# Optimization experiments

Measured on AMD Instinct MI355X. Metric: run time of the kernel, lower is better.

Reference implementation:

```python
import jax, jax.numpy as jnp
import numpy as np
from functools import partial

NX, NY = 48, 48
LX, LY = 1.0, 1.0
T, DT = 0.01, 0.0001
NT = int(T / DT)  # 100 sequential explicit-Euler steps
DX, DY = LX / NX, LY / NY
TWO_PI = 2.0 * jnp.pi


def setup_inputs() -> dict:
    key = jax.random.key(0)
    u0 = jax.random.normal(key, (8192, 1, NX, NY), dtype=jnp.float32)
    return {
        "u0": u0,
        "alpha_w1": jnp.float32(0.1),
        "alpha_w2": jnp.float32(0.1),
        "alpha_w3": jnp.float32(0.1),
        "beta_w1": jnp.float32(0.3),
        "beta_w2": jnp.float32(0.2),
        "beta_w3": jnp.float32(0.1),
    }


def _coeff_grids(a1, a2, a3, b1, b2, b3):
    x = jnp.linspace(0.0, LX, NX)
    y = jnp.linspace(0.0, LY, NY)
    yy, xx = jnp.meshgrid(y, x, indexing="ij")  # (NY, NX), matches torch.meshgrid(y, x, 'ij')
    alpha = 0.5 * DT * (jnp.abs(a1) + jnp.abs(a2) * jnp.sin(TWO_PI * yy)
                        + jnp.abs(a3) * jnp.cos(TWO_PI * yy)) / DX ** 2
    beta = DT * (jnp.abs(b1) + jnp.abs(b2) * jnp.cos(TWO_PI * xx)
                 + jnp.abs(b3) * jnp.sin(TWO_PI * xx)) / DY ** 2
    return alpha[None], beta[None]  # (1, NY, NX) broadcast over batch (square grid)


def reference(u0, alpha_w1, alpha_w2, alpha_w3, beta_w1, beta_w2, beta_w3):
    alpha_grid, beta_grid = _coeff_grids(alpha_w1, alpha_w2, alpha_w3,
                                         beta_w1, beta_w2, beta_w3)
    u = u0[:, 0]  # (B, NX, NY)
    # reflect-pad once; the boundary ring stays frozen across all timesteps
    u = jnp.pad(u, ((0, 0), (1, 1), (1, 1)), mode="reflect")

    def step(u, _):
        ui = u[:, 1:-1, 1:-1]
        u_xx = u[:, 2:, 1:-1] - 2.0 * ui + u[:, :-2, 1:-1]
        u_yy = u[:, 1:-1, 2:] - 2.0 * ui + u[:, 1:-1, :-2]
        u = u.at[:, 1:-1, 1:-1].set(ui + alpha_grid * u_xx + beta_grid * u_yy)
        return u, None

    u, _ = jax.lax.scan(step, u, None, length=NT)
    return u[:, 1:-1, 1:-1][:, None]  # (B, 1, NX, NY)
```

## Files before the change

kernel.cpp:

```cpp
#include <hip/hip_runtime.h>
#include <hip/hip_fp16.h>
#include <math.h>


#define NTSTEPS 100

typedef __half2 h2;

__device__ __forceinline__ h2 dpp_row_shr1(h2 oldv, h2 x) {
    int r = __builtin_amdgcn_update_dpp(
        __builtin_bit_cast(int, oldv), __builtin_bit_cast(int, x),
        0x111, 0xF, 0xF, false);
    return __builtin_bit_cast(h2, r);
}
__device__ __forceinline__ h2 dpp_row_shl1(h2 oldv, h2 x) {
    int r = __builtin_amdgcn_update_dpp(
        __builtin_bit_cast(int, oldv), __builtin_bit_cast(int, x),
        0x101, 0xF, 0xF, false);
    return __builtin_bit_cast(h2, r);
}
__device__ __forceinline__ h2 bperm(int addr, h2 x) {
    int r = __builtin_amdgcn_ds_bpermute(addr, __builtin_bit_cast(int, x));
    return __builtin_bit_cast(h2, r);
}

__global__ void coeff_kernel(
    const float* __restrict__ pa1, const float* __restrict__ pa2,
    const float* __restrict__ pa3, const float* __restrict__ pb1,
    const float* __restrict__ pb2, const float* __restrict__ pb3,
    float* __restrict__ ws)
{
    int tid = threadIdx.x;
    if (tid < 48) {
        float a1 = fabsf(pa1[0]), a2 = fabsf(pa2[0]), a3 = fabsf(pa3[0]);
        float b1 = fabsf(pb1[0]), b2 = fabsf(pb2[0]), b3 = fabsf(pb3[0]);
        float t = 6.283185307179586f * ((float)tid / 47.0f);
        float s = sinf(t), c = cosf(t);
        ws[tid]      = 0.1152f * (a1 + a2 * s + a3 * c);
        ws[48 + tid] = 0.2304f * (b1 + b2 * c + b3 * s);
    }
}

__global__ __launch_bounds__(256) void pde_kernel(
    const float* __restrict__ u0,
    const float* __restrict__ cw,
    float* __restrict__ out)
{
    const int tid  = threadIdx.x;
    const int lane = tid & 63;
    const int wv   = tid >> 6;
    const int pair = blockIdx.x * 4 + wv;
    const int tx   = lane & 15;
    const int ty   = lane >> 4;
    const int c0   = 3 * tx;
    const int r0   = 12 * ty;

    const float* __restrict__ srcA = u0 + (size_t)(2 * pair) * 2304;
    const float* __restrict__ srcB = srcA + 2304;

    h2 a[12], b[3];
    #pragma unroll
    for (int k = 0; k < 12; ++k) a[k] = __half2half2(__float2half(cw[r0 + k]));
    #pragma unroll
    for (int c = 0; c < 3; ++c) b[c] = __half2half2(__float2half(cw[48 + c0 + c]));
    const h2 neg2 = __floats2half2_rn(-2.0f, -2.0f);

    h2 u[12][3];
    h2 ep[12];
    h2 tH[3], bH[3];

    const int epc = (tx == 15) ? 46 : 1;
    #pragma unroll
    for (int k = 0; k < 12; ++k) {
        #pragma unroll
        for (int c = 0; c < 3; ++c) {
            int o = (r0 + k) * 48 + c0 + c;
            u[k][c] = __floats2half2_rn(srcA[o], srcB[o]);
        }
        int oe = (r0 + k) * 48 + epc;
        ep[k] = __floats2half2_rn(srcA[oe], srcB[oe]);
    }
    {
        const int tor = (ty == 0) ? 1 : (r0 - 1);
        const int bor = (ty == 3) ? 46 : (r0 + 12);
        #pragma unroll
        for (int c = 0; c < 3; ++c) {
            int ot = tor * 48 + c0 + c, ob = bor * 48 + c0 + c;
            tH[c] = __floats2half2_rn(srcA[ot], srcB[ot]);
            bH[c] = __floats2half2_rn(srcA[ob], srcB[ob]);
        }
    }

    const int upA = ((lane - 16) & 63) << 2;
    const int dnA = ((lane + 16) & 63) << 2;
    const bool notTop = (ty != 0);
    const bool notBot = (ty != 3);

    #pragma unroll 1
    for (int t = 0; t < NTSTEPS; ++t) {
        #pragma unroll
        for (int c = 0; c < 3; ++c) {
            h2 tv = bperm(upA, u[11][c]);
            h2 bv = bperm(dnA, u[0][c]);
            tH[c] = notTop ? tv : tH[c];
            bH[c] = notBot ? bv : bH[c];
        }
        h2 p0 = tH[0], p1 = tH[1], p2 = tH[2];
        #pragma unroll
        for (int k = 0; k < 12; ++k) {
            const h2 x0 = u[k][0], x1 = u[k][1], x2 = u[k][2];
            const h2 hl = dpp_row_shr1(ep[k], x2);
            const h2 hr = dpp_row_shl1(ep[k], x0);
            const h2 d0 = (k == 11) ? bH[0] : u[k + 1][0];
            const h2 d1 = (k == 11) ? bH[1] : u[k + 1][1];
            const h2 d2 = (k == 11) ? bH[2] : u[k + 1][2];
            const h2 s10 = __hadd2(p0, d0);
            const h2 s11 = __hadd2(p1, d1);
            const h2 s12 = __hadd2(p2, d2);
            const h2 s20 = __hadd2(hl, x1);
            const h2 s21 = __hadd2(x0, x2);
            const h2 s22 = __hadd2(x1, hr);
            const h2 t10 = __hfma2(neg2, x0, s10);
            const h2 t11 = __hfma2(neg2, x1, s11);
            const h2 t12 = __hfma2(neg2, x2, s12);
            const h2 t20 = __hfma2(neg2, x0, s20);
            const h2 t21 = __hfma2(neg2, x1, s21);
            const h2 t22 = __hfma2(neg2, x2, s22);
            const h2 n0 = __hfma2(b[0], t20, __hfma2(a[k], t10, x0));
            const h2 n1 = __hfma2(b[1], t21, __hfma2(a[k], t11, x1));
            const h2 n2 = __hfma2(b[2], t22, __hfma2(a[k], t12, x2));
            p0 = x0; p1 = x1; p2 = x2;
            u[k][0] = n0; u[k][1] = n1; u[k][2] = n2;
        }
    }

    float* __restrict__ dstA = out + (size_t)(2 * pair) * 2304;
    float* __restrict__ dstB = dstA + 2304;
    #pragma unroll
    for (int k = 0; k < 12; ++k) {
        #pragma unroll
        for (int c = 0; c < 3; ++c) {
            int o = (r0 + k) * 48 + c0 + c;
            dstA[o] = __low2float(u[k][c]);
            dstB[o] = __high2float(u[k][c]);
        }
    }
}

extern "C" void kernel_launch(void* const* d_in, const int* in_sizes, int n_in,
                              void* d_out, int out_size, void* d_ws, size_t ws_size,
                              hipStream_t stream) {
    const float* u0 = (const float*)d_in[0];
    float* ws = (float*)d_ws;
    coeff_kernel<<<1, 64, 0, stream>>>(
        (const float*)d_in[1], (const float*)d_in[2], (const float*)d_in[3],
        (const float*)d_in[4], (const float*)d_in[5], (const float*)d_in[6],
        ws);
    pde_kernel<<<1024, 256, 0, stream>>>(u0, ws, (float*)d_out);
}
```

Baseline: 335.7 us.

## Fold stencil diagonal into precomputed coefficients and overlap halo exchange with interior rows

Each update is rewritten as cc*x + a*(up+down) + b*(left+right), with the diagonal coefficient 1-2a-2b precomputed per cell. This removes the two -2x FMAs per row group. The frozen left and right boundary contributions are folded into per-row additive terms, so the DPP shifts can use zero-fill instead of old values. Boundary rows 0 and 11 are computed first and their ds_bpermute halo exchange is issued before the interior rows, hiding LDS-permute latency behind the interior arithmetic. The cost is more register pressure from the cc, e0 and e2 arrays, and changed fp16 rounding.

```diff
diff --git a/kernel.cpp b/kernel.cpp
--- a/kernel.cpp
+++ b/kernel.cpp
@@ -7,16 +7,14 @@
 
 typedef __half2 h2;
 
-__device__ __forceinline__ h2 dpp_row_shr1(h2 oldv, h2 x) {
+__device__ __forceinline__ h2 dpp_shr1_z(h2 x) {
     int r = __builtin_amdgcn_update_dpp(
-        __builtin_bit_cast(int, oldv), __builtin_bit_cast(int, x),
-        0x111, 0xF, 0xF, false);
+        0, __builtin_bit_cast(int, x), 0x111, 0xF, 0xF, true);
     return __builtin_bit_cast(h2, r);
 }
-__device__ __forceinline__ h2 dpp_row_shl1(h2 oldv, h2 x) {
+__device__ __forceinline__ h2 dpp_shl1_z(h2 x) {
     int r = __builtin_amdgcn_update_dpp(
-        __builtin_bit_cast(int, oldv), __builtin_bit_cast(int, x),
-        0x101, 0xF, 0xF, false);
+        0, __builtin_bit_cast(int, x), 0x101, 0xF, 0xF, true);
     return __builtin_bit_cast(h2, r);
 }
 __device__ __forceinline__ h2 bperm(int addr, h2 x) {
@@ -41,6 +39,21 @@
     }
 }
 
+#define ROWSTEP(K, UP0, UP1, UP2, DN0, DN1, DN2, X0, X1, X2, N0, N1, N2)      \
+    do {                                                                      \
+        const h2 hl  = dpp_shr1_z(X2);                                        \
+        const h2 hr  = dpp_shl1_z(X0);                                        \
+        const h2 s10 = __hadd2(UP0, DN0);                                     \
+        const h2 s11 = __hadd2(UP1, DN1);                                     \
+        const h2 s12 = __hadd2(UP2, DN2);                                     \
+        const h2 s20 = __hadd2(hl, X1);                                       \
+        const h2 s21 = __hadd2(X0, X2);                                       \
+        const h2 s22 = __hadd2(X1, hr);                                       \
+        N0 = __hfma2(a[K], s10, __hfma2(b0, s20, __hfma2(cc[K][0], X0, e0[K]))); \
+        N1 = __hfma2(a[K], s11, __hfma2(b1, s21, __hmul2(cc[K][1], X1)));     \
+        N2 = __hfma2(a[K], s12, __hfma2(b2, s22, __hfma2(cc[K][2], X2, e2[K]))); \
+    } while (0)
+
 __global__ __launch_bounds__(256) void pde_kernel(
     const float* __restrict__ u0,
     const float* __restrict__ cw,
@@ -58,17 +71,29 @@
     const float* __restrict__ srcA = u0 + (size_t)(2 * pair) * 2304;
     const float* __restrict__ srcB = srcA + 2304;
 
-    h2 a[12], b[3];
+    float bf0 = cw[48 + c0 + 0];
+    float bf1 = cw[48 + c0 + 1];
+    float bf2 = cw[48 + c0 + 2];
+    const h2 b0 = __half2half2(__float2half(bf0));
+    const h2 b1 = __half2half2(__float2half(bf1));
+    const h2 b2 = __half2half2(__float2half(bf2));
+
+    h2 a[12], cc[12][3];
     #pragma unroll
-    for (int k = 0; k < 12; ++k) a[k] = __half2half2(__float2half(cw[r0 + k]));
-    #pragma unroll
-    for (int c = 0; c < 3; ++c) b[c] = __half2half2(__float2half(cw[48 + c0 + c]));
-    const h2 neg2 = __floats2half2_rn(-2.0f, -2.0f);
+    for (int k = 0; k < 12; ++k) {
+        float av = cw[r0 + k];
+        a[k] = __half2half2(__float2half(av));
+        cc[k][0] = __half2half2(__float2half(1.0f - 2.0f * av - 2.0f * bf0));
+        cc[k][1] = __half2half2(__float2half(1.0f - 2.0f * av - 2.0f * bf1));
+        cc[k][2] = __half2half2(__float2half(1.0f - 2.0f * av - 2.0f * bf2));
+    }
 
     h2 u[12][3];
-    h2 ep[12];
+    h2 e0[12], e2[12];
     h2 tH[3], bH[3];
+    h2 tF[3], bF[3];
 
+    const h2 hz = __floats2half2_rn(0.0f, 0.0f);
     const int epc = (tx == 15) ? 46 : 1;
     #pragma unroll
     for (int k = 0; k < 12; ++k) {
@@ -78,7 +103,9 @@
             u[k][c] = __floats2half2_rn(srcA[o], srcB[o]);
         }
         int oe = (r0 + k) * 48 + epc;
-        ep[k] = __floats2half2_rn(srcA[oe], srcB[oe]);
+        float eA = srcA[oe], eB = srcB[oe];
+        e0[k] = (tx == 0)  ? __floats2half2_rn(bf0 * eA, bf0 * eB) : hz;
+        e2[k] = (tx == 15) ? __floats2half2_rn(bf2 * eA, bf2 * eB) : hz;
     }
     {
         const int tor = (ty == 0) ? 1 : (r0 - 1);
@@ -88,6 +115,8 @@
             int ot = tor * 48 + c0 + c, ob = bor * 48 + c0 + c;
             tH[c] = __floats2half2_rn(srcA[ot], srcB[ot]);
             bH[c] = __floats2half2_rn(srcA[ob], srcB[ob]);
+            tF[c] = tH[c];
+            bF[c] = bH[c];
         }
     }
 
@@ -98,39 +127,46 @@
 
     #pragma unroll 1
     for (int t = 0; t < NTSTEPS; ++t) {
+        h2 n0, n1, n2;
+        const h2 x110 = u[11][0], x111 = u[11][1], x112 = u[11][2];
+        ROWSTEP(11, u[10][0], u[10][1], u[10][2], bH[0], bH[1], bH[2],
+                x110, x111, x112, n0, n1, n2);
+        u[11][0] = n0; u[11][1] = n1; u[11][2] = n2;
+
+        h2 p0 = u[0][0], p1 = u[0][1], p2 = u[0][2];
+        ROWSTEP(0, tH[0], tH[1], tH[2], u[1][0], u[1][1], u[1][2],
+                p0, p1, p2, n0, n1, n2);
+        u[0][0] = n0; u[0][1] = n1; u[0][2] = n2;
+
+        const bool more = (t + 1 < NTSTEPS);
+        h2 rT0, rT1, rT2, rB0, rB1, rB2;
+        if (more) {
+            rT0 = bperm(upA, u[11][0]);
+            rT1 = bperm(upA, u[11][1]);
+            rT2 = bperm(upA, u[11][2]);
+            rB0 = bperm(dnA, u[0][0]);
+            rB1 = bperm(dnA, u[0][1]);
+            rB2 = bperm(dnA, u[0][2]);
+        }
+
         #pragma unroll
-        for (int c = 0; c < 3; ++c) {
-            h2 tv = bperm(upA, u[11][c]);
-            h2 bv = bperm(dnA, u[0][c]);
-            tH[c] = notTop ? tv : tH[c];
-            bH[c] = notBot ? bv : bH[c];
+        for (int k = 1; k <= 10; ++k) {
+            const h2 q0 = u[k][0], q1 = u[k][1], q2 = u[k][2];
+            const h2 d0 = (k == 10) ? x110 : u[k + 1][0];
+            const h2 d1 = (k == 10) ? x111 : u[k + 1][1];
+            const h2 d2 = (k == 10) ? x112 : u[k + 1][2];
+            ROWSTEP(k, p0, p1, p2, d0, d1, d2, q0, q1, q2, n0, n1, n2);
+            u[k][0] = n0; u[k][1] = n1; u[k][2] = n2;
+            p0 = q0; p1 = q1; p2 = q2;
         }
-        h2 p0 = tH[0], p1 = tH[1], p2 = tH[2];
-        #pragma unroll
-        for (int k = 0; k < 12; ++k) {
-            const h2 x0 = u[k][0], x1 = u[k][1], x2 = u[k][2];
-            const h2 hl = dpp_row_shr1(ep[k], x2);
-            const h2 hr = dpp_row_shl1(ep[k], x0);
-            const h2 d0 = (k == 11) ? bH[0] : u[k + 1][0];
-            const h2 d1 = (k == 11) ? bH[1] : u[k + 1][1];
-            const h2 d2 = (k == 11) ? bH[2] : u[k + 1][2];
-            const h2 s10 = __hadd2(p0, d0);
-            const h2 s11 = __hadd2(p1, d1);
-            const h2 s12 = __hadd2(p2, d2);
-            const h2 s20 = __hadd2(hl, x1);
-            const h2 s21 = __hadd2(x0, x2);
-            const h2 s22 = __hadd2(x1, hr);
-            const h2 t10 = __hfma2(neg2, x0, s10);
-            const h2 t11 = __hfma2(neg2, x1, s11);
-            const h2 t12 = __hfma2(neg2, x2, s12);
-            const h2 t20 = __hfma2(neg2, x0, s20);
-            const h2 t21 = __hfma2(neg2, x1, s21);
-            const h2 t22 = __hfma2(neg2, x2, s22);
-            const h2 n0 = __hfma2(b[0], t20, __hfma2(a[k], t10, x0));
-            const h2 n1 = __hfma2(b[1], t21, __hfma2(a[k], t11, x1));
-            const h2 n2 = __hfma2(b[2], t22, __hfma2(a[k], t12, x2));
-            p0 = x0; p1 = x1; p2 = x2;
-            u[k][0] = n0; u[k][1] = n1; u[k][2] = n2;
+
+        if (more) {
+            tH[0] = notTop ? rT0 : tF[0];
+            tH[1] = notTop ? rT1 : tF[1];
+            tH[2] = notTop ? rT2 : tF[2];
+            bH[0] = notBot ? rB0 : bF[0];
+            bH[1] = notBot ? rB1 : bF[1];
+            bH[2] = notBot ? rB2 : bF[2];
         }
     }
 
```

Result: faster. 300.4 us (-10.5%).
